# Performance work log

Measured on AMD Instinct MI355X. Metric: run time of the kernel, lower is better.

## Reference

```python
import math
import jax, jax.numpy as jnp
import numpy as np

NUM_HEADS = 16
D_MODEL = 1024
D_HEAD = 64
D_SEQ = 2048
NUM_LAYERS = 24
BATCH = 2


def setup_inputs() -> dict:
    key = jax.random.key(0)
    ks = jax.random.split(key, 10)
    s = math.sqrt(0.02)
    residual = jax.random.normal(ks[0], (BATCH, D_SEQ, D_MODEL), dtype=jnp.float32)
    W_Q = jax.random.normal(ks[1], (NUM_HEADS, D_MODEL, D_HEAD), dtype=jnp.float32) * s
    W_K = jax.random.normal(ks[2], (NUM_HEADS, D_MODEL, D_HEAD), dtype=jnp.float32) * s
    W_V = jax.random.normal(ks[3], (NUM_HEADS, D_MODEL, D_HEAD), dtype=jnp.float32) * s
    W_O = jax.random.normal(ks[4], (NUM_HEADS * D_HEAD, D_MODEL), dtype=jnp.float32) * s
    W_O = W_O / math.sqrt(NUM_LAYERS)
    b_Q = jax.random.normal(ks[5], (NUM_HEADS, D_HEAD), dtype=jnp.float32) * s
    b_K = jax.random.normal(ks[6], (NUM_HEADS, D_HEAD), dtype=jnp.float32) * s
    b_V = jax.random.normal(ks[7], (NUM_HEADS, D_HEAD), dtype=jnp.float32) * s
    b_O = jax.random.normal(ks[8], (D_MODEL,), dtype=jnp.float32) * s
    return dict(residual=residual, W_Q=W_Q, W_K=W_K, W_V=W_V, W_O=W_O,
                b_Q=b_Q, b_K=b_K, b_V=b_V, b_O=b_O)


def reference(residual, W_Q, W_K, W_V, W_O, b_Q, b_K, b_V, b_O):
    # residual: [b, s, m]; W_{Q,K,V}: [h, m, d]; b_{Q,K,V}: [h, d]
    Q = jnp.einsum('hmd,bsm->bshd', W_Q, residual) + b_Q
    K = jnp.einsum('hmd,bsm->bshd', W_K, residual) + b_K
    V = jnp.einsum('hmd,bsm->bshd', W_V, residual) + b_V
    # full causal score matrix [b, h, s_q, s_k], masked with -inf above diagonal
    QK = jnp.einsum('bqhd,bkhd->bhqk', Q, K)
    seq = residual.shape[1]
    causal = jnp.triu(jnp.ones((seq, seq), dtype=bool), k=1)  # True above diag
    QK_masked = jnp.where(causal, -jnp.inf, QK)
    soft = jax.nn.softmax(QK_masked / math.sqrt(D_HEAD), axis=-1)
    attn = jnp.einsum('bhqk,bkhd->bqhd', soft, V)  # [b, s, h, d]
    multi_head = attn.reshape(attn.shape[0], attn.shape[1], NUM_HEADS * D_HEAD)
    return jnp.einsum('em,bqe->bqm', W_O, multi_head) + b_O
```

## Files before the change

kernel.cpp:

```cpp
#include <hip/hip_runtime.h>
#include <stdint.h>

typedef unsigned short u16;
typedef unsigned long long u64;
typedef _Float16 f16;
typedef __attribute__((ext_vector_type(8))) _Float16 f16x8;
typedef __attribute__((ext_vector_type(4))) float f32x4;
typedef __attribute__((ext_vector_type(16))) float f32x16;
typedef __attribute__((ext_vector_type(4))) unsigned short u16x4;
typedef __attribute__((ext_vector_type(8))) unsigned short u16x8;

#define NHEADS 16
#define DMODEL 1024
#define DHEAD 64
#define SEQ 2048
#define NBATCH 2
#define MROWS (NBATCH * SEQ)
#define NQKV 3072
#define SCQ 0.18033688011112042f

__device__ __forceinline__ u16 f2h(float x) {
  union { f16 h; u16 u; } v;
  v.h = (f16)x;
  return v.u;
}

__device__ __forceinline__ unsigned pk2u(float x, float y) {
  typedef __fp16 fp16x2 __attribute__((ext_vector_type(2)));
  fp16x2 h = __builtin_amdgcn_cvt_pkrtz(x, y);
  union { fp16x2 h; unsigned u; } v; v.h = h;
  return v.u;
}

__device__ __forceinline__ f16x8 mkfrag(unsigned w0, unsigned w1, unsigned w2, unsigned w3) {
  union { unsigned u[4]; f16x8 f; } t;
  t.u[0] = w0; t.u[1] = w1; t.u[2] = w2; t.u[3] = w3;
  return t.f;
}

__device__ __forceinline__ f16x8 vfrag(const char* row, int sz, int F, int hib8) {
  union { u64 u[2]; f16x8 f; } t;
  t.u[0] = *(const u64*)(row + (((2 * F) ^ sz) << 4) + hib8);
  t.u[1] = *(const u64*)(row + (((2 * F + 1) ^ sz) << 4) + hib8);
  return t.f;
}

__device__ __forceinline__ void gload_lds16(const void* g, void* l) {
  __builtin_amdgcn_global_load_lds(
      (const __attribute__((address_space(1))) void*)g,
      (__attribute__((address_space(3))) void*)l, 16, 0, 0);
}

__global__ __launch_bounds__(256) void prep_kernel(
    const float* __restrict__ X,
    const float* __restrict__ WQ, const float* __restrict__ WK,
    const float* __restrict__ WV, const float* __restrict__ WO,
    u16* __restrict__ Xh, u16* __restrict__ Wqkv, u16* __restrict__ Wo) {
  __shared__ u16 lt[64][72];
  int blk = blockIdx.x;
  if (blk < 2048) {
    int i = blk * 256 + threadIdx.x;
    const f32x4* xv = (const f32x4*)(X + (size_t)i * 8);
    f32x4 a = xv[0], b = xv[1];
    u16x8 o;
    o[0] = f2h(a[0]); o[1] = f2h(a[1]); o[2] = f2h(a[2]); o[3] = f2h(a[3]);
    o[4] = f2h(b[0]); o[5] = f2h(b[1]); o[6] = f2h(b[2]); o[7] = f2h(b[3]);
    *(u16x8*)(Xh + (size_t)i * 8) = o;
  } else if (blk < 2816) {
    int bb = blk - 2048;
    int mt = bb & 15, hh = (bb >> 4) & 15, qkv = bb >> 8;
    const float* W = (qkv == 0) ? WQ : (qkv == 1) ? WK : WV;
    int m_in = threadIdx.x >> 2, dq = threadIdx.x & 3;
    const f32x4* sp4 = (const f32x4*)(W + (size_t)hh * (DMODEL * DHEAD) +
                                      (size_t)(mt * 64 + m_in) * DHEAD + dq * 16);
#pragma unroll
    for (int v4 = 0; v4 < 4; ++v4) {
      f32x4 a = sp4[v4];
#pragma unroll
      for (int j = 0; j < 4; ++j) lt[dq * 16 + v4 * 4 + j][m_in] = f2h(a[j]);
    }
    __syncthreads();
    int d_in = threadIdx.x >> 2, mq = threadIdx.x & 3;
    size_t orow = ((size_t)(qkv * 1024 + hh * 64 + d_in)) * DMODEL + mt * 64 + mq * 16;
    u16x8 o0, o1;
#pragma unroll
    for (int j = 0; j < 8; ++j) {
      o0[j] = lt[d_in][mq * 16 + j];
      o1[j] = lt[d_in][mq * 16 + 8 + j];
    }
    *(u16x8*)(Wqkv + orow) = o0;
    *(u16x8*)(Wqkv + orow + 8) = o1;
  } else {
    int bb = blk - 2816;
    int mt = bb & 15, et = bb >> 4;
    int e_in = threadIdx.x >> 2, mq = threadIdx.x & 3;
    const f32x4* sp4 = (const f32x4*)(WO + (size_t)(et * 64 + e_in) * DMODEL + mt * 64 + mq * 16);
#pragma unroll
    for (int v4 = 0; v4 < 4; ++v4) {
      f32x4 a = sp4[v4];
#pragma unroll
      for (int j = 0; j < 4; ++j) lt[mq * 16 + v4 * 4 + j][e_in] = f2h(a[j]);
    }
    __syncthreads();
    int m_in = threadIdx.x >> 2, eq = threadIdx.x & 3;
    size_t orow = (size_t)(mt * 64 + m_in) * DMODEL + et * 64 + eq * 16;
    u16x8 o0, o1;
#pragma unroll
    for (int j = 0; j < 8; ++j) {
      o0[j] = lt[m_in][eq * 16 + j];
      o1[j] = lt[m_in][eq * 16 + 8 + j];
    }
    *(u16x8*)(Wo + orow) = o0;
    *(u16x8*)(Wo + orow + 8) = o1;
  }
}

__global__ __launch_bounds__(256, 2) void gemm_qkv(
    const u16* __restrict__ A, const u16* __restrict__ Bt,
    const float* __restrict__ bq, const float* __restrict__ bk, const float* __restrict__ bv,
    u16* __restrict__ Qo, u16* __restrict__ Ko, u16* __restrict__ Vto) {
  __shared__ u16 lds[2][8192];
  const int tid = threadIdx.x;
  const int wid = tid >> 6, lane = tid & 63, lr = lane & 15, lg = lane >> 4;
  const int wr = wid >> 1, wc = wid & 1;
  const int brow = blockIdx.y * 128, bcol = blockIdx.x * 128;

  f32x4 acc[4][4];
#pragma unroll
  for (int i = 0; i < 4; ++i)
#pragma unroll
    for (int j = 0; j < 4; ++j) acc[i][j] = (f32x4){0.f, 0.f, 0.f, 0.f};

#define STAGE(buf, kt)                                                               \
  {                                                                                  \
    _Pragma("unroll") for (int i = 0; i < 2; ++i) {                                  \
      int idx = tid + i * 256;                                                       \
      gload_lds16(A + (size_t)(brow + (idx >> 2)) * 1024 + (kt) * 32 + (idx & 3) * 8,\
                  (char*)&lds[buf][0] + (wid * 64 + i * 256) * 16);                  \
    }                                                                                \
    _Pragma("unroll") for (int i = 0; i < 2; ++i) {                                  \
      int idx = tid + i * 256;                                                       \
      gload_lds16(Bt + (size_t)(bcol + (idx >> 2)) * 1024 + (kt) * 32 + (idx & 3) * 8,\
                  (char*)&lds[buf][4096] + (wid * 64 + i * 256) * 16);               \
    }                                                                                \
  }

  STAGE(0, 0);
  __syncthreads();
  int cur = 0;
  for (int kt = 0; kt < 32; ++kt) {
    if (kt + 1 < 32) STAGE(cur ^ 1, kt + 1);
    const u16* Ab = &lds[cur][0];
    const u16* Bb = &lds[cur][4096];
    f16x8 a[4], b[4];
#pragma unroll
    for (int ar = 0; ar < 4; ++ar)
      a[ar] = *(const f16x8*)(Ab + (wr * 64 + ar * 16 + lr) * 32 + lg * 8);
#pragma unroll
    for (int bc = 0; bc < 4; ++bc)
      b[bc] = *(const f16x8*)(Bb + (wc * 64 + bc * 16 + lr) * 32 + lg * 8);
#pragma unroll
    for (int ar = 0; ar < 4; ++ar)
#pragma unroll
      for (int bc = 0; bc < 4; ++bc)
        acc[ar][bc] = __builtin_amdgcn_mfma_f32_16x16x32_f16(a[ar], b[bc], acc[ar][bc], 0, 0, 0);
    __syncthreads();
    cur ^= 1;
  }

#pragma unroll
  for (int ar = 0; ar < 4; ++ar) {
    int row0 = brow + wr * 64 + ar * 16 + lg * 4;
    int bb = row0 >> 11, s0 = row0 & 2047;
#pragma unroll
    for (int bc = 0; bc < 4; ++bc) {
      int n = bcol + wc * 64 + bc * 16 + lr;
      int qkv = n >> 10, hd = n & 1023, h = hd >> 6, d = hd & 63;
      float bias = ((qkv == 0) ? bq : (qkv == 1) ? bk : bv)[hd];
      if (qkv < 2) {
        u16* dst = qkv ? Ko : Qo;
        float sc = qkv ? 1.f : SCQ;
        size_t base = ((size_t)(bb * NHEADS + h) * SEQ + s0) * DHEAD + d;
#pragma unroll
        for (int r = 0; r < 4; ++r)
          dst[base + (size_t)r * DHEAD] = f2h((acc[ar][bc][r] + bias) * sc);
      } else {
        u16x4 o;
        o[0] = f2h(acc[ar][bc][0] + bias);
        o[1] = f2h(acc[ar][bc][1] + bias);
        o[2] = f2h(acc[ar][bc][2] + bias);
        o[3] = f2h(acc[ar][bc][3] + bias);
        *(u16x4*)(Vto + ((size_t)(bb * NHEADS + h) * DHEAD + d) * SEQ + s0) = o;
      }
    }
  }
}

__global__ __launch_bounds__(256, 2) void gemm_out(
    const u16* __restrict__ A, const u16* __restrict__ Bt,
    const float* __restrict__ bo, float* __restrict__ Co) {
  __shared__ u16 lds[2][8192];
  const int tid = threadIdx.x;
  const int wid = tid >> 6, lane = tid & 63, lr = lane & 15, lg = lane >> 4;
  const int wr = wid >> 1, wc = wid & 1;
  const int brow = blockIdx.y * 128, bcol = blockIdx.x * 128;

  f32x4 acc[4][4];
#pragma unroll
  for (int i = 0; i < 4; ++i)
#pragma unroll
    for (int j = 0; j < 4; ++j) acc[i][j] = (f32x4){0.f, 0.f, 0.f, 0.f};

  STAGE(0, 0);
  __syncthreads();
  int cur = 0;
  for (int kt = 0; kt < 32; ++kt) {
    if (kt + 1 < 32) STAGE(cur ^ 1, kt + 1);
    const u16* Ab = &lds[cur][0];
    const u16* Bb = &lds[cur][4096];
    f16x8 a[4], b[4];
#pragma unroll
    for (int ar = 0; ar < 4; ++ar)
      a[ar] = *(const f16x8*)(Ab + (wr * 64 + ar * 16 + lr) * 32 + lg * 8);
#pragma unroll
    for (int bc = 0; bc < 4; ++bc)
      b[bc] = *(const f16x8*)(Bb + (wc * 64 + bc * 16 + lr) * 32 + lg * 8);
#pragma unroll
    for (int ar = 0; ar < 4; ++ar)
#pragma unroll
      for (int bc = 0; bc < 4; ++bc)
        acc[ar][bc] = __builtin_amdgcn_mfma_f32_16x16x32_f16(a[ar], b[bc], acc[ar][bc], 0, 0, 0);
    __syncthreads();
    cur ^= 1;
  }
#undef STAGE

#pragma unroll
  for (int ar = 0; ar < 4; ++ar) {
    int row0 = brow + wr * 64 + ar * 16 + lg * 4;
#pragma unroll
    for (int bc = 0; bc < 4; ++bc) {
      int n = bcol + wc * 64 + bc * 16 + lr;
      float bias = bo[n];
#pragma unroll
      for (int r = 0; r < 4; ++r)
        Co[(size_t)(row0 + r) * DMODEL + n] = acc[ar][bc][r] + bias;
    }
  }
}

__global__ __launch_bounds__(256, 2) void attn_kernel(
    const u16* __restrict__ Q, const u16* __restrict__ K,
    const u16* __restrict__ Vt, u16* __restrict__ MH) {
  __shared__ char sh8[32768];
  const int tid = threadIdx.x, wid = tid >> 6, lane = tid & 63;
  const int l31 = lane & 31, hi = lane >> 5;
  const int bid = blockIdx.x;
  const int half = bid >> 8;
  const int u = bid & 255;
  const int jj = u >> 4;
  const int j = half ? (15 - jj) : jj;
  const int bh = (u & 15) + 16 * half;
  const int h = bh & 15, b = bh >> 4;
  const int nt = 2 * j + 2;
  const int tw = 2 * j + 1 + (wid >> 1);
  const u16* Qb = Q + (size_t)bh * (SEQ * DHEAD);
  const u16* Kb = K + (size_t)bh * (SEQ * DHEAD);
  const u16* Vb = Vt + (size_t)bh * (DHEAD * SEQ);

#pragma unroll
  for (int i = 0; i < 4; ++i) {
    int idx = tid + i * 256, row = idx >> 3;
    int sseg = (idx & 7) ^ ((row ^ (row >> 3)) & 7);
    char* qdst = (idx < 512) ? sh8 + 8192 + idx * 16 : sh8 + 24576 + (idx - 512) * 16;
    gload_lds16(Qb + (size_t)(128 * j + row) * DHEAD + sseg * 8, qdst);
  }
#pragma unroll
  for (int i = 0; i < 2; ++i) {
    int idx = tid + i * 256, row = idx >> 3;
    int sseg = (idx & 7) ^ ((row ^ (row >> 3)) & 7);
    gload_lds16(Kb + (size_t)row * DHEAD + sseg * 8, sh8 + idx * 16);
    gload_lds16(Vb + (size_t)row * SEQ + sseg * 8, sh8 + 16384 + idx * 16);
  }
  __syncthreads();

  f16x8 qf0, qf1, qf2, qf3;
  {
    int row = ((wid & 1) << 5) + l31;
    int swz = ((row ^ (row >> 3)) & 7) << 4;
    const char* qb = sh8 + ((wid < 2) ? 8192 : 24576) + row * 128;
    qf0 = *(const f16x8*)(qb + ((hi * 16 + 0)  ^ swz));
    qf1 = *(const f16x8*)(qb + ((hi * 16 + 32) ^ swz));
    qf2 = *(const f16x8*)(qb + ((hi * 16 + 64) ^ swz));
    qf3 = *(const f16x8*)(qb + ((hi * 16 + 96) ^ swz));
  }
  __syncthreads();

  f32x16 acc0, acc1;
#pragma unroll
  for (int z = 0; z < 16; ++z) { acc0[z] = 0.f; acc1[z] = 0.f; }
  float m = -1e30f, l = 0.f;
  const int qa = 128 * j + (wid << 5) + l31;

  const int sw0 = (l31 ^ (l31 >> 3)) & 7;
  const int kz0 = sw0 << 4;
  const int r32 = 32 + l31;
  const int sw1 = (r32 ^ (r32 >> 3)) & 7;
  const int kz1 = sw1 << 4;
  const int hib = hi * 16;
  const int hib8 = hi * 8;

  for (int kt = 0; kt < nt; ++kt) {
    if (kt + 1 < nt) {
      const int kb_n = ((kt + 1) & 1) ? 8192 : 0;
      const int vb_n = ((kt + 1) & 1) ? 24576 : 16384;
#pragma unroll
      for (int i = 0; i < 2; ++i) {
        int idx = tid + i * 256, rw = idx >> 3;
        int sseg = (idx & 7) ^ ((rw ^ (rw >> 3)) & 7);
        gload_lds16(Kb + (size_t)((kt + 1) * 64 + rw) * DHEAD + sseg * 8, sh8 + kb_n + idx * 16);
        gload_lds16(Vb + (size_t)rw * SEQ + (kt + 1) * 64 + sseg * 8, sh8 + vb_n + idx * 16);
      }
    }
    const bool act = (kt < tw);
    const bool dg = (kt == tw - 1);

    if (act) {
      const char* kbuf = sh8 + ((kt & 1) ? 8192 : 0);
      const char* vbuf = sh8 + ((kt & 1) ? 24576 : 16384);

      f32x16 s0, s1;
#pragma unroll
      for (int z = 0; z < 16; ++z) { s0[z] = 0.f; s1[z] = 0.f; }
      {
        const char* kb0 = kbuf + l31 * 128;
        const char* kb1 = kbuf + r32 * 128;
        f16x8 kf;
        __builtin_amdgcn_s_setprio(1);
        kf = *(const f16x8*)(kb0 + ((hib + 0)  ^ kz0)); s0 = __builtin_amdgcn_mfma_f32_32x32x16_f16(kf, qf0, s0, 0, 0, 0);
        kf = *(const f16x8*)(kb0 + ((hib + 32) ^ kz0)); s0 = __builtin_amdgcn_mfma_f32_32x32x16_f16(kf, qf1, s0, 0, 0, 0);
        kf = *(const f16x8*)(kb0 + ((hib + 64) ^ kz0)); s0 = __builtin_amdgcn_mfma_f32_32x32x16_f16(kf, qf2, s0, 0, 0, 0);
        kf = *(const f16x8*)(kb0 + ((hib + 96) ^ kz0)); s0 = __builtin_amdgcn_mfma_f32_32x32x16_f16(kf, qf3, s0, 0, 0, 0);
        kf = *(const f16x8*)(kb1 + ((hib + 0)  ^ kz1)); s1 = __builtin_amdgcn_mfma_f32_32x32x16_f16(kf, qf0, s1, 0, 0, 0);
        kf = *(const f16x8*)(kb1 + ((hib + 32) ^ kz1)); s1 = __builtin_amdgcn_mfma_f32_32x32x16_f16(kf, qf1, s1, 0, 0, 0);
        kf = *(const f16x8*)(kb1 + ((hib + 64) ^ kz1)); s1 = __builtin_amdgcn_mfma_f32_32x32x16_f16(kf, qf2, s1, 0, 0, 0);
        kf = *(const f16x8*)(kb1 + ((hib + 96) ^ kz1)); s1 = __builtin_amdgcn_mfma_f32_32x32x16_f16(kf, qf3, s1, 0, 0, 0);
        __builtin_amdgcn_s_setprio(0);
      }

      if (dg) {
#pragma unroll
        for (int rr = 0; rr < 16; ++rr) {
          int k0 = kt * 64 + (rr & 3) + 8 * (rr >> 2) + 4 * hi;
          if (k0 > qa) s0[rr] = -1e30f;
          if (k0 + 32 > qa) s1[rr] = -1e30f;
        }
      }

      float tm = s0[0];
#pragma unroll
      for (int rr = 1; rr < 16; ++rr) tm = fmaxf(tm, s0[rr]);
#pragma unroll
      for (int rr = 0; rr < 16; ++rr) tm = fmaxf(tm, s1[rr]);
      tm = fmaxf(tm, __shfl_xor(tm, 32));

      if (!__all(tm <= m + 8.f)) {
        float m2 = fmaxf(m, tm);
        float al = exp2f(m - m2);
        m = m2;
        l *= al;
#pragma unroll
        for (int rr = 0; rr < 16; ++rr) {
          int qp = (rr & 3) + 8 * (rr >> 2) + 4 * hi;
          float af = __shfl(al, qp);
          acc0[rr] *= af;
          acc1[rr] *= af;
        }
      }

      float rs = 0.f;
#pragma unroll
      for (int rr = 0; rr < 16; ++rr) { s0[rr] = exp2f(s0[rr] - m); rs += s0[rr]; }
#pragma unroll
      for (int rr = 0; rr < 16; ++rr) { s1[rr] = exp2f(s1[rr] - m); rs += s1[rr]; }
      rs += __shfl_xor(rs, 32);
      l += rs;

      f16x8 pa0 = mkfrag(pk2u(s0[0],  s0[1]),  pk2u(s0[2],  s0[3]),
                         pk2u(s0[4],  s0[5]),  pk2u(s0[6],  s0[7]));
      f16x8 pa1 = mkfrag(pk2u(s0[8],  s0[9]),  pk2u(s0[10], s0[11]),
                         pk2u(s0[12], s0[13]), pk2u(s0[14], s0[15]));
      f16x8 pa2 = mkfrag(pk2u(s1[0],  s1[1]),  pk2u(s1[2],  s1[3]),
                         pk2u(s1[4],  s1[5]),  pk2u(s1[6],  s1[7]));
      f16x8 pa3 = mkfrag(pk2u(s1[8],  s1[9]),  pk2u(s1[10], s1[11]),
                         pk2u(s1[12], s1[13]), pk2u(s1[14], s1[15]));

      {
        const char* vr0 = vbuf + l31 * 128;
        const char* vr1 = vbuf + r32 * 128;
        __builtin_amdgcn_s_setprio(1);
        acc0 = __builtin_amdgcn_mfma_f32_32x32x16_f16(pa0, vfrag(vr0, sw0, 0, hib8), acc0, 0, 0, 0);
        acc0 = __builtin_amdgcn_mfma_f32_32x32x16_f16(pa1, vfrag(vr0, sw0, 1, hib8), acc0, 0, 0, 0);
        acc0 = __builtin_amdgcn_mfma_f32_32x32x16_f16(pa2, vfrag(vr0, sw0, 2, hib8), acc0, 0, 0, 0);
        acc0 = __builtin_amdgcn_mfma_f32_32x32x16_f16(pa3, vfrag(vr0, sw0, 3, hib8), acc0, 0, 0, 0);
        acc1 = __builtin_amdgcn_mfma_f32_32x32x16_f16(pa0, vfrag(vr1, sw1, 0, hib8), acc1, 0, 0, 0);
        acc1 = __builtin_amdgcn_mfma_f32_32x32x16_f16(pa1, vfrag(vr1, sw1, 1, hib8), acc1, 0, 0, 0);
        acc1 = __builtin_amdgcn_mfma_f32_32x32x16_f16(pa2, vfrag(vr1, sw1, 2, hib8), acc1, 0, 0, 0);
        acc1 = __builtin_amdgcn_mfma_f32_32x32x16_f16(pa3, vfrag(vr1, sw1, 3, hib8), acc1, 0, 0, 0);
        __builtin_amdgcn_s_setprio(0);
      }

      if (dg) {
#pragma unroll
        for (int rr = 0; rr < 16; ++rr) {
          int qp = (rr & 3) + 8 * (rr >> 2) + 4 * hi;
          float ls = __shfl(l, qp);
          int qrow = 128 * j + (wid << 5) + qp;
          size_t base = ((size_t)(b * SEQ) + qrow) * DMODEL + h * DHEAD;
          MH[base + l31]      = f2h(acc0[rr] / ls);
          MH[base + 32 + l31] = f2h(acc1[rr] / ls);
        }
      }
    }

    __syncthreads();
  }
}

extern "C" void kernel_launch(void* const* d_in, const int* in_sizes, int n_in,
                              void* d_out, int out_size, void* d_ws, size_t ws_size,
                              hipStream_t stream) {
  const float* residual = (const float*)d_in[0];
  const float* WQ = (const float*)d_in[1];
  const float* WK = (const float*)d_in[2];
  const float* WV = (const float*)d_in[3];
  const float* WO = (const float*)d_in[4];
  const float* bQ = (const float*)d_in[5];
  const float* bK = (const float*)d_in[6];
  const float* bV = (const float*)d_in[7];
  const float* bO = (const float*)d_in[8];
  float* out = (float*)d_out;

  char* w = (char*)d_ws;
  u16* Xh   = (u16*)(w);
  u16* Wqkv = (u16*)(w + ((size_t)8 << 20));
  u16* Wo   = (u16*)(w + ((size_t)14 << 20));
  u16* Qd   = (u16*)(w + ((size_t)16 << 20));
  u16* Kd   = (u16*)(w + ((size_t)24 << 20));
  u16* Vtd  = (u16*)(w + ((size_t)32 << 20));
  u16* MH   = (u16*)(w + ((size_t)40 << 20));

  prep_kernel<<<3072, 256, 0, stream>>>(residual, WQ, WK, WV, WO, Xh, Wqkv, Wo);

  gemm_qkv<<<dim3(NQKV / 128, MROWS / 128), 256, 0, stream>>>(
      Xh, Wqkv, bQ, bK, bV, Qd, Kd, Vtd);

  attn_kernel<<<512, 256, 0, stream>>>(Qd, Kd, Vtd, MH);

  gemm_out<<<dim3(DMODEL / 128, MROWS / 128), 256, 0, stream>>>(MH, Wo, bO, out);
}
```

Baseline: 125.1 us.

## Split KV range across wave pairs and pair complementary 64-row query tiles per block

Each attention block now handles two 64-row query tiles (t and 31-t) for causal load balance. Within a block the two wave pairs split the key tiles between them instead of sharing them, then merge partial softmax states (m, l, acc) through shared memory. LDS doubles to 64 KB to hold two stages of double-buffered K/V, and each pair processes alternate key tiles. This aims to cut the wasted masked work of the old 128-row tiles and balance per-block work, but the larger LDS footprint may reduce occupancy and the merge adds extra syncs.

```diff
diff --git a/kernel.cpp b/kernel.cpp
--- a/kernel.cpp
+++ b/kernel.cpp
@@ -252,178 +252,216 @@
 __global__ __launch_bounds__(256, 2) void attn_kernel(
     const u16* __restrict__ Q, const u16* __restrict__ K,
     const u16* __restrict__ Vt, u16* __restrict__ MH) {
-  __shared__ char sh8[32768];
+  __shared__ char sh8[65536];
   const int tid = threadIdx.x, wid = tid >> 6, lane = tid & 63;
   const int l31 = lane & 31, hi = lane >> 5;
+  const int pairid = wid >> 1;
+  const int qsub = wid & 1;
   const int bid = blockIdx.x;
-  const int half = bid >> 8;
-  const int u = bid & 255;
-  const int jj = u >> 4;
-  const int j = half ? (15 - jj) : jj;
-  const int bh = (u & 15) + 16 * half;
+  const int p = bid >> 5, bh = bid & 31;
   const int h = bh & 15, b = bh >> 4;
-  const int nt = 2 * j + 2;
-  const int tw = 2 * j + 1 + (wid >> 1);
+  const int tA = 31 - p, tB = p;
   const u16* Qb = Q + (size_t)bh * (SEQ * DHEAD);
   const u16* Kb = K + (size_t)bh * (SEQ * DHEAD);
   const u16* Vb = Vt + (size_t)bh * (DHEAD * SEQ);
 
-#pragma unroll
-  for (int i = 0; i < 4; ++i) {
-    int idx = tid + i * 256, row = idx >> 3;
-    int sseg = (idx & 7) ^ ((row ^ (row >> 3)) & 7);
-    char* qdst = (idx < 512) ? sh8 + 8192 + idx * 16 : sh8 + 24576 + (idx - 512) * 16;
-    gload_lds16(Qb + (size_t)(128 * j + row) * DHEAD + sseg * 8, qdst);
-  }
+  const int sw0 = (l31 ^ (l31 >> 3)) & 7, kz0 = sw0 << 4;
+  const int r32 = 32 + l31;
+  const int sw1 = (r32 ^ (r32 >> 3)) & 7, kz1 = sw1 << 4;
+  const int hib = hi * 16, hib8 = hi * 8;
+
 #pragma unroll
   for (int i = 0; i < 2; ++i) {
     int idx = tid + i * 256, row = idx >> 3;
     int sseg = (idx & 7) ^ ((row ^ (row >> 3)) & 7);
+    gload_lds16(Qb + (size_t)(tA * 64 + row) * DHEAD + sseg * 8, sh8 + 32768 + idx * 16);
+    gload_lds16(Qb + (size_t)(tB * 64 + row) * DHEAD + sseg * 8, sh8 + 40960 + idx * 16);
     gload_lds16(Kb + (size_t)row * DHEAD + sseg * 8, sh8 + idx * 16);
     gload_lds16(Vb + (size_t)row * SEQ + sseg * 8, sh8 + 16384 + idx * 16);
+    gload_lds16(Kb + (size_t)(64 + row) * DHEAD + sseg * 8, sh8 + 8192 + idx * 16);
+    gload_lds16(Vb + (size_t)row * SEQ + 64 + sseg * 8, sh8 + 24576 + idx * 16);
   }
   __syncthreads();
 
-  f16x8 qf0, qf1, qf2, qf3;
+  f16x8 qfA0, qfA1, qfA2, qfA3, qfB0, qfB1, qfB2, qfB3;
   {
-    int row = ((wid & 1) << 5) + l31;
+    int row = (qsub << 5) + l31;
     int swz = ((row ^ (row >> 3)) & 7) << 4;
-    const char* qb = sh8 + ((wid < 2) ? 8192 : 24576) + row * 128;
-    qf0 = *(const f16x8*)(qb + ((hi * 16 + 0)  ^ swz));
-    qf1 = *(const f16x8*)(qb + ((hi * 16 + 32) ^ swz));
-    qf2 = *(const f16x8*)(qb + ((hi * 16 + 64) ^ swz));
-    qf3 = *(const f16x8*)(qb + ((hi * 16 + 96) ^ swz));
+    const char* qa = sh8 + 32768 + row * 128;
+    const char* qb = sh8 + 40960 + row * 128;
+    qfA0 = *(const f16x8*)(qa + ((hib + 0)  ^ swz));
+    qfA1 = *(const f16x8*)(qa + ((hib + 32) ^ swz));
+    qfA2 = *(const f16x8*)(qa + ((hib + 64) ^ swz));
+    qfA3 = *(const f16x8*)(qa + ((hib + 96) ^ swz));
+    qfB0 = *(const f16x8*)(qb + ((hib + 0)  ^ swz));
+    qfB1 = *(const f16x8*)(qb + ((hib + 32) ^ swz));
+    qfB2 = *(const f16x8*)(qb + ((hib + 64) ^ swz));
+    qfB3 = *(const f16x8*)(qb + ((hib + 96) ^ swz));
   }
   __syncthreads();
 
-  f32x16 acc0, acc1;
-#pragma unroll
-  for (int z = 0; z < 16; ++z) { acc0[z] = 0.f; acc1[z] = 0.f; }
-  float m = -1e30f, l = 0.f;
-  const int qa = 128 * j + (wid << 5) + l31;
-
-  const int sw0 = (l31 ^ (l31 >> 3)) & 7;
-  const int kz0 = sw0 << 4;
-  const int r32 = 32 + l31;
-  const int sw1 = (r32 ^ (r32 >> 3)) & 7;
-  const int kz1 = sw1 << 4;
-  const int hib = hi * 16;
-  const int hib8 = hi * 8;
-
-  for (int kt = 0; kt < nt; ++kt) {
-    if (kt + 1 < nt) {
-      const int kb_n = ((kt + 1) & 1) ? 8192 : 0;
-      const int vb_n = ((kt + 1) & 1) ? 24576 : 16384;
+#pragma unroll
+  for (int seg = 0; seg < 2; ++seg) {
+    const int t = seg ? tB : tA;
+    const f16x8 q0f = seg ? qfB0 : qfA0;
+    const f16x8 q1f = seg ? qfB1 : qfA1;
+    const f16x8 q2f = seg ? qfB2 : qfA2;
+    const f16x8 q3f = seg ? qfB3 : qfA3;
+
+    if (seg == 1) {
 #pragma unroll
       for (int i = 0; i < 2; ++i) {
-        int idx = tid + i * 256, rw = idx >> 3;
-        int sseg = (idx & 7) ^ ((rw ^ (rw >> 3)) & 7);
-        gload_lds16(Kb + (size_t)((kt + 1) * 64 + rw) * DHEAD + sseg * 8, sh8 + kb_n + idx * 16);
-        gload_lds16(Vb + (size_t)rw * SEQ + (kt + 1) * 64 + sseg * 8, sh8 + vb_n + idx * 16);
+        int idx = tid + i * 256, row = idx >> 3;
+        int sseg = (idx & 7) ^ ((row ^ (row >> 3)) & 7);
+        gload_lds16(Kb + (size_t)row * DHEAD + sseg * 8, sh8 + idx * 16);
+        gload_lds16(Vb + (size_t)row * SEQ + sseg * 8, sh8 + 16384 + idx * 16);
+        if (t >= 1) {
+          gload_lds16(Kb + (size_t)(64 + row) * DHEAD + sseg * 8, sh8 + 8192 + idx * 16);
+          gload_lds16(Vb + (size_t)row * SEQ + 64 + sseg * 8, sh8 + 24576 + idx * 16);
+        }
       }
-    }
-    const bool act = (kt < tw);
-    const bool dg = (kt == tw - 1);
-
-    if (act) {
-      const char* kbuf = sh8 + ((kt & 1) ? 8192 : 0);
-      const char* vbuf = sh8 + ((kt & 1) ? 24576 : 16384);
-
-      f32x16 s0, s1;
-#pragma unroll
-      for (int z = 0; z < 16; ++z) { s0[z] = 0.f; s1[z] = 0.f; }
-      {
-        const char* kb0 = kbuf + l31 * 128;
-        const char* kb1 = kbuf + r32 * 128;
-        f16x8 kf;
-        __builtin_amdgcn_s_setprio(1);
-        kf = *(const f16x8*)(kb0 + ((hib + 0)  ^ kz0)); s0 = __builtin_amdgcn_mfma_f32_32x32x16_f16(kf, qf0, s0, 0, 0, 0);
-        kf = *(const f16x8*)(kb0 + ((hib + 32) ^ kz0)); s0 = __builtin_amdgcn_mfma_f32_32x32x16_f16(kf, qf1, s0, 0, 0, 0);
-        kf = *(const f16x8*)(kb0 + ((hib + 64) ^ kz0)); s0 = __builtin_amdgcn_mfma_f32_32x32x16_f16(kf, qf2, s0, 0, 0, 0);
-        kf = *(const f16x8*)(kb0 + ((hib + 96) ^ kz0)); s0 = __builtin_amdgcn_mfma_f32_32x32x16_f16(kf, qf3, s0, 0, 0, 0);
-        kf = *(const f16x8*)(kb1 + ((hib + 0)  ^ kz1)); s1 = __builtin_amdgcn_mfma_f32_32x32x16_f16(kf, qf0, s1, 0, 0, 0);
-        kf = *(const f16x8*)(kb1 + ((hib + 32) ^ kz1)); s1 = __builtin_amdgcn_mfma_f32_32x32x16_f16(kf, qf1, s1, 0, 0, 0);
-        kf = *(const f16x8*)(kb1 + ((hib + 64) ^ kz1)); s1 = __builtin_amdgcn_mfma_f32_32x32x16_f16(kf, qf2, s1, 0, 0, 0);
-        kf = *(const f16x8*)(kb1 + ((hib + 96) ^ kz1)); s1 = __builtin_amdgcn_mfma_f32_32x32x16_f16(kf, qf3, s1, 0, 0, 0);
-        __builtin_amdgcn_s_setprio(0);
+      __syncthreads();
+    }
+
+    f32x16 acc0, acc1;
+#pragma unroll
+    for (int z = 0; z < 16; ++z) { acc0[z] = 0.f; acc1[z] = 0.f; }
+    float m = -1e30f, l = 0.f;
+    const int qg = t * 64 + (qsub << 5) + l31;
+    const int wall = (t >> 1) + 1;
+
+    for (int si = 0; si < wall; ++si) {
+      const int off = (si & 1) ? 32768 : 0;
+      const int offn = off ^ 32768;
+      const int e = 2 * si + 2;
+      if (e <= t) {
+#pragma unroll
+        for (int i = 0; i < 2; ++i) {
+          int idx = tid + i * 256, row = idx >> 3;
+          int sseg = (idx & 7) ^ ((row ^ (row >> 3)) & 7);
+          gload_lds16(Kb + (size_t)(e * 64 + row) * DHEAD + sseg * 8, sh8 + offn + idx * 16);
+          gload_lds16(Vb + (size_t)row * SEQ + e * 64 + sseg * 8, sh8 + offn + 16384 + idx * 16);
+          if (e + 1 <= t) {
+            gload_lds16(Kb + (size_t)((e + 1) * 64 + row) * DHEAD + sseg * 8,
+                        sh8 + offn + 8192 + idx * 16);
+            gload_lds16(Vb + (size_t)row * SEQ + (e + 1) * 64 + sseg * 8,
+                        sh8 + offn + 24576 + idx * 16);
+          }
+        }
       }
-
-      if (dg) {
-#pragma unroll
-        for (int rr = 0; rr < 16; ++rr) {
-          int k0 = kt * 64 + (rr & 3) + 8 * (rr >> 2) + 4 * hi;
-          if (k0 > qa) s0[rr] = -1e30f;
-          if (k0 + 32 > qa) s1[rr] = -1e30f;
+      const int kt = 2 * si + pairid;
+      if (kt <= t) {
+        const char* kbuf = sh8 + off + pairid * 8192;
+        const char* vbuf = sh8 + off + 16384 + pairid * 8192;
+
+        f32x16 s0, s1;
+#pragma unroll
+        for (int z = 0; z < 16; ++z) { s0[z] = 0.f; s1[z] = 0.f; }
+        {
+          const char* kb0 = kbuf + l31 * 128;
+          const char* kb1 = kbuf + r32 * 128;
+          f16x8 kf;
+          __builtin_amdgcn_s_setprio(1);
+          kf = *(const f16x8*)(kb0 + ((hib + 0)  ^ kz0)); s0 = __builtin_amdgcn_mfma_f32_32x32x16_f16(kf, q0f, s0, 0, 0, 0);
+          kf = *(const f16x8*)(kb0 + ((hib + 32) ^ kz0)); s0 = __builtin_amdgcn_mfma_f32_32x32x16_f16(kf, q1f, s0, 0, 0, 0);
+          kf = *(const f16x8*)(kb0 + ((hib + 64) ^ kz0)); s0 = __builtin_amdgcn_mfma_f32_32x32x16_f16(kf, q2f, s0, 0, 0, 0);
+          kf = *(const f16x8*)(kb0 + ((hib + 96) ^ kz0)); s0 = __builtin_amdgcn_mfma_f32_32x32x16_f16(kf, q3f, s0, 0, 0, 0);
+          kf = *(const f16x8*)(kb1 + ((hib + 0)  ^ kz1)); s1 = __builtin_amdgcn_mfma_f32_32x32x16_f16(kf, q0f, s1, 0, 0, 0);
+          kf = *(const f16x8*)(kb1 + ((hib + 32) ^ kz1)); s1 = __builtin_amdgcn_mfma_f32_32x32x16_f16(kf, q1f, s1, 0, 0, 0);
+          kf = *(const f16x8*)(kb1 + ((hib + 64) ^ kz1)); s1 = __builtin_amdgcn_mfma_f32_32x32x16_f16(kf, q2f, s1, 0, 0, 0);
+          kf = *(const f16x8*)(kb1 + ((hib + 96) ^ kz1)); s1 = __builtin_amdgcn_mfma_f32_32x32x16_f16(kf, q3f, s1, 0, 0, 0);
+          __builtin_amdgcn_s_setprio(0);
+        }
+
+        if (kt == t) {
+#pragma unroll
+          for (int rr = 0; rr < 16; ++rr) {
+            int k0 = kt * 64 + (rr & 3) + 8 * (rr >> 2) + 4 * hi;
+            if (k0 > qg) s0[rr] = -1e30f;
+            if (k0 + 32 > qg) s1[rr] = -1e30f;
+          }
+        }
+
+        float tm = s0[0];
+#pragma unroll
+        for (int rr = 1; rr < 16; ++rr) tm = fmaxf(tm, s0[rr]);
+#pragma unroll
+        for (int rr = 0; rr < 16; ++rr) tm = fmaxf(tm, s1[rr]);
+        tm = fmaxf(tm, __shfl_xor(tm, 32));
+
+        if (!__all(tm <= m + 8.f)) {
+          float m2 = fmaxf(m, tm);
+          float al = exp2f(m - m2);
+          m = m2;
+          l *= al;
+#pragma unroll
+          for (int rr = 0; rr < 16; ++rr) {
+            int qp = (rr & 3) + 8 * (rr >> 2) + 4 * hi;
+            float af = __shfl(al, qp);
+            acc0[rr] *= af;
+            acc1[rr] *= af;
+          }
+        }
+
+        float rs = 0.f;
+#pragma unroll
+        for (int rr = 0; rr < 16; ++rr) { s0[rr] = exp2f(s0[rr] - m); rs += s0[rr]; }
+#pragma unroll
+        for (int rr = 0; rr < 16; ++rr) { s1[rr] = exp2f(s1[rr] - m); rs += s1[rr]; }
+        rs += __shfl_xor(rs, 32);
+        l += rs;
+
+        f16x8 pa0 = mkfrag(pk2u(s0[0],  s0[1]),  pk2u(s0[2],  s0[3]),
+                           pk2u(s0[4],  s0[5]),  pk2u(s0[6],  s0[7]));
+        f16x8 pa1 = mkfrag(pk2u(s0[8],  s0[9]),  pk2u(s0[10], s0[11]),
+                           pk2u(s0[12], s0[13]), pk2u(s0[14], s0[15]));
+        f16x8 pa2 = mkfrag(pk2u(s1[0],  s1[1]),  pk2u(s1[2],  s1[3]),
+                           pk2u(s1[4],  s1[5]),  pk2u(s1[6],  s1[7]));
+        f16x8 pa3 = mkfrag(pk2u(s1[8],  s1[9]),  pk2u(s1[10], s1[11]),
+                           pk2u(s1[12], s1[13]), pk2u(s1[14], s1[15]));
+
+        {
+          const char* vr0 = vbuf + l31 * 128;
+          const char* vr1 = vbuf + r32 * 128;
+          __builtin_amdgcn_s_setprio(1);
+          acc0 = __builtin_amdgcn_mfma_f32_32x32x16_f16(pa0, vfrag(vr0, sw0, 0, hib8), acc0, 0, 0, 0);
+          acc0 = __builtin_amdgcn_mfma_f32_32x32x16_f16(pa1, vfrag(vr0, sw0, 1, hib8), acc0, 0, 0, 0);
+          acc0 = __builtin_amdgcn_mfma_f32_32x32x16_f16(pa2, vfrag(vr0, sw0, 2, hib8), acc0, 0, 0, 0);
+          acc0 = __builtin_amdgcn_mfma_f32_32x32x16_f16(pa3, vfrag(vr0, sw0, 3, hib8), acc0, 0, 0, 0);
+          acc1 = __builtin_amdgcn_mfma_f32_32x32x16_f16(pa0, vfrag(vr1, sw1, 0, hib8), acc1, 0, 0, 0);
+          acc1 = __builtin_amdgcn_mfma_f32_32x32x16_f16(pa1, vfrag(vr1, sw1, 1, hib8), acc1, 0, 0, 0);
+          acc1 = __builtin_amdgcn_mfma_f32_32x32x16_f16(pa2, vfrag(vr1, sw1, 2, hib8), acc1, 0, 0, 0);
+          acc1 = __builtin_amdgcn_mfma_f32_32x32x16_f16(pa3, vfrag(vr1, sw1, 3, hib8), acc1, 0, 0, 0);
+          __builtin_amdgcn_s_setprio(0);
         }
       }
-
-      float tm = s0[0];
-#pragma unroll
-      for (int rr = 1; rr < 16; ++rr) tm = fmaxf(tm, s0[rr]);
-#pragma unroll
-      for (int rr = 0; rr < 16; ++rr) tm = fmaxf(tm, s1[rr]);
-      tm = fmaxf(tm, __shfl_xor(tm, 32));
-
-      if (!__all(tm <= m + 8.f)) {
-        float m2 = fmaxf(m, tm);
-        float al = exp2f(m - m2);
-        m = m2;
-        l *= al;
-#pragma unroll
-        for (int rr = 0; rr < 16; ++rr) {
-          int qp = (rr & 3) + 8 * (rr >> 2) + 4 * hi;
-          float af = __shfl(al, qp);
-          acc0[rr] *= af;
-          acc1[rr] *= af;
-        }
+      __syncthreads();
+    }
+
+    {
+      const int slot = (qsub << 6) | (hi << 5) | l31;
+      float* z = (float*)(sh8 + (pairid ? 16384 : 0)) + slot * 18;
+      z[0] = m; z[1] = l;
+#pragma unroll
+      for (int rr = 0; rr < 16; ++rr) z[2 + rr] = pairid ? acc0[rr] : acc1[rr];
+      __syncthreads();
+      const float* y = (const float*)(sh8 + (pairid ? 0 : 16384)) + slot * 18;
+      float mb = y[0], lb = y[1];
+      float mM = fmaxf(m, mb);
+      float aw = exp2f(m - mM), bw = exp2f(mb - mM);
+      float lM = l * aw + lb * bw;
+      const int d = pairid ? (32 + l31) : l31;
+#pragma unroll
+      for (int rr = 0; rr < 16; ++rr) {
+        int qp = (rr & 3) + 8 * (rr >> 2) + 4 * hi;
+        float aF = __shfl(aw, qp), bF = __shfl(bw, qp), lF = __shfl(lM, qp);
+        float own = pairid ? acc1[rr] : acc0[rr];
+        float val = (own * aF + y[2 + rr] * bF) / lF;
+        int q = t * 64 + (qsub << 5) + qp;
+        MH[((size_t)(b * SEQ) + q) * DMODEL + h * DHEAD + d] = f2h(val);
       }
-
-      float rs = 0.f;
-#pragma unroll
-      for (int rr = 0; rr < 16; ++rr) { s0[rr] = exp2f(s0[rr] - m); rs += s0[rr]; }
-#pragma unroll
-      for (int rr = 0; rr < 16; ++rr) { s1[rr] = exp2f(s1[rr] - m); rs += s1[rr]; }
-      rs += __shfl_xor(rs, 32);
-      l += rs;
-
-      f16x8 pa0 = mkfrag(pk2u(s0[0],  s0[1]),  pk2u(s0[2],  s0[3]),
-                         pk2u(s0[4],  s0[5]),  pk2u(s0[6],  s0[7]));
-      f16x8 pa1 = mkfrag(pk2u(s0[8],  s0[9]),  pk2u(s0[10], s0[11]),
-                         pk2u(s0[12], s0[13]), pk2u(s0[14], s0[15]));
-      f16x8 pa2 = mkfrag(pk2u(s1[0],  s1[1]),  pk2u(s1[2],  s1[3]),
-                         pk2u(s1[4],  s1[5]),  pk2u(s1[6],  s1[7]));
-      f16x8 pa3 = mkfrag(pk2u(s1[8],  s1[9]),  pk2u(s1[10], s1[11]),
-                         pk2u(s1[12], s1[13]), pk2u(s1[14], s1[15]));
-
-      {
-        const char* vr0 = vbuf + l31 * 128;
-        const char* vr1 = vbuf + r32 * 128;
-        __builtin_amdgcn_s_setprio(1);
-        acc0 = __builtin_amdgcn_mfma_f32_32x32x16_f16(pa0, vfrag(vr0, sw0, 0, hib8), acc0, 0, 0, 0);
-        acc0 = __builtin_amdgcn_mfma_f32_32x32x16_f16(pa1, vfrag(vr0, sw0, 1, hib8), acc0, 0, 0, 0);
-        acc0 = __builtin_amdgcn_mfma_f32_32x32x16_f16(pa2, vfrag(vr0, sw0, 2, hib8), acc0, 0, 0, 0);
-        acc0 = __builtin_amdgcn_mfma_f32_32x32x16_f16(pa3, vfrag(vr0, sw0, 3, hib8), acc0, 0, 0, 0);
-        acc1 = __builtin_amdgcn_mfma_f32_32x32x16_f16(pa0, vfrag(vr1, sw1, 0, hib8), acc1, 0, 0, 0);
-        acc1 = __builtin_amdgcn_mfma_f32_32x32x16_f16(pa1, vfrag(vr1, sw1, 1, hib8), acc1, 0, 0, 0);
-        acc1 = __builtin_amdgcn_mfma_f32_32x32x16_f16(pa2, vfrag(vr1, sw1, 2, hib8), acc1, 0, 0, 0);
-        acc1 = __builtin_amdgcn_mfma_f32_32x32x16_f16(pa3, vfrag(vr1, sw1, 3, hib8), acc1, 0, 0, 0);
-        __builtin_amdgcn_s_setprio(0);
-      }
-
-      if (dg) {
-#pragma unroll
-        for (int rr = 0; rr < 16; ++rr) {
-          int qp = (rr & 3) + 8 * (rr >> 2) + 4 * hi;
-          float ls = __shfl(l, qp);
-          int qrow = 128 * j + (wid << 5) + qp;
-          size_t base = ((size_t)(b * SEQ) + qrow) * DMODEL + h * DHEAD;
-          MH[base + l31]      = f2h(acc0[rr] / ls);
-          MH[base + 32 + l31] = f2h(acc1[rr] / ls);
-        }
-      }
-    }
-
-    __syncthreads();
+      __syncthreads();
+    }
   }
 }
 
```

Result: faster. 117.3 us (-6.3%).
